# Performance work log

Hardware: AMD Instinct MI355X
Metric: run time of the kernel (lower is better)

The kernel has to match this reference:

```python
import jax, jax.numpy as jnp
import numpy as np

D = 512    # d_model == EMBED_DIM
H = 8      # nhead
FF = 2048  # dim_feedforward
T, B, S, M = 64, 32, 64, 256
EPS = 1e-5


def setup_inputs() -> dict:
    key = jax.random.key(0)
    ks = iter(jax.random.split(key, 40))
    rn = lambda k, shp, s=0.02: s * jax.random.normal(k, shp, jnp.float32)
    inp = {
        'tgt': jax.random.normal(next(ks), (T, B, D), jnp.float32),
        'memory': jax.random.normal(next(ks), (M, B, D), jnp.float32),
        'semantics': jax.random.normal(next(ks), (B, S, D), jnp.float32),
    }
    for pfx in ('pt', 'sa', 'ca'):  # pre_target, self_attn, cross multihead_attn
        inp[pfx + '_wqkv'] = rn(next(ks), (3 * D, D))
        inp[pfx + '_bqkv'] = jnp.zeros((3 * D,), jnp.float32)
        inp[pfx + '_wo'] = rn(next(ks), (D, D))
        inp[pfx + '_bo'] = jnp.zeros((D,), jnp.float32)
    # relevant_mlp_pre_target: fc0 (2D->D), relu, fc1 (D->D), relu, fc2 (D->1)
    inp['mlp_w0'] = rn(next(ks), (D, 2 * D), float(np.sqrt(2.0 / (2 * D))))
    inp['mlp_b0'] = jnp.zeros((D,), jnp.float32)
    inp['mlp_w1'] = rn(next(ks), (D, D), float(np.sqrt(2.0 / D)))
    inp['mlp_b1'] = jnp.zeros((D,), jnp.float32)
    inp['mlp_w2'] = rn(next(ks), (1, D), float(np.sqrt(2.0 / D)))
    inp['mlp_b2'] = jnp.zeros((1,), jnp.float32)
    inp['ffn_w1'] = rn(next(ks), (FF, D))
    inp['ffn_b1'] = jnp.zeros((FF,), jnp.float32)
    inp['ffn_w2'] = rn(next(ks), (D, FF))
    inp['ffn_b2'] = jnp.zeros((D,), jnp.float32)
    for i in (1, 2, 3):
        inp[f'ln{i}_g'] = jnp.ones((D,), jnp.float32)
        inp[f'ln{i}_b'] = jnp.zeros((D,), jnp.float32)
    return inp


def layernorm(x, g, b):
    mu = jnp.mean(x, -1, keepdims=True)
    var = jnp.var(x, -1, keepdims=True)
    return (x - mu) * jax.lax.rsqrt(var + EPS) * g + b


def mha(q, k, v, wqkv, bqkv, wo, bo):
    # q,k,v: (L, B, D) seq-first, like torch nn.MultiheadAttention
    hd = D // H
    wq, wk, wv = jnp.split(wqkv, 3, axis=0)
    bq, bk, bv = jnp.split(bqkv, 3)
    qh = (q @ wq.T + bq).reshape(q.shape[0], q.shape[1], H, hd)
    kh = (k @ wk.T + bk).reshape(k.shape[0], k.shape[1], H, hd)
    vh = (v @ wv.T + bv).reshape(v.shape[0], v.shape[1], H, hd)
    scale = 1.0 / float(np.sqrt(hd))
    att = jax.nn.softmax(jnp.einsum('qbhd,kbhd->bhqk', qh * scale, kh), axis=-1)
    out = jnp.einsum('bhqk,kbhd->qbhd', att, vh).reshape(q.shape[0], q.shape[1], D)
    return out @ wo.T + bo


def get_relevant_semantic(feats, sem, w0, b0, w1, b1, w2, b2):
    # feats: (B,T,D), sem: (B,S,D). Linear-on-concat == sum of two linears, so we
    # never materialize the (B,T,S,2D) cat tensor; hidden (B,T,S,D) is unavoidable math.
    w0c, w0s = w0[:, :D], w0[:, D:]
    h = (feats @ w0c.T)[:, :, None, :] + (sem @ w0s.T)[:, None, :, :] + b0  # (B,T,S,D)
    h = jax.nn.relu(h)
    h = jax.nn.relu(h @ w1.T + b1)
    scores = h @ w2.T + b2                      # (B,T,S,1)
    a = jax.nn.softmax(scores, axis=2)          # softmax over sem axis
    return jnp.sum(sem[:, None, :, :] * a, axis=2)  # (B,T,D)


def reference(tgt, memory, semantics,
              pt_wqkv, pt_bqkv, pt_wo, pt_bo,
              sa_wqkv, sa_bqkv, sa_wo, sa_bo,
              ca_wqkv, ca_bqkv, ca_wo, ca_bo,
              mlp_w0, mlp_b0, mlp_w1, mlp_b1, mlp_w2, mlp_b2,
              ffn_w1, ffn_b1, ffn_w2, ffn_b2,
              ln1_g, ln1_b, ln2_g, ln2_b, ln3_g, ln3_b):
    # MULTIHEAD_PRE_TARGET branch (eval mode: dropout = identity)
    rel = get_relevant_semantic(jnp.transpose(tgt, (1, 0, 2)), semantics,
                                mlp_w0, mlp_b0, mlp_w1, mlp_b1, mlp_w2, mlp_b2)
    sem_k = jnp.transpose(rel, (1, 0, 2))  # (T,B,D) seq-first key/value
    x = tgt + mha(tgt, sem_k, sem_k, pt_wqkv, pt_bqkv, pt_wo, pt_bo)
    # self attention
    x = layernorm(x + mha(x, x, x, sa_wqkv, sa_bqkv, sa_wo, sa_bo), ln1_g, ln1_b)
    # cross attention over encoder memory
    x = layernorm(x + mha(x, memory, memory, ca_wqkv, ca_bqkv, ca_wo, ca_bo), ln2_g, ln2_b)
    # feed-forward
    ff = jax.nn.relu(x @ ffn_w1.T + ffn_b1) @ ffn_w2.T + ffn_b2
    return layernorm(x + ff, ln3_g, ln3_b)
```

## Files before the change

kernel.cpp:

```cpp
#include <hip/hip_runtime.h>
#include <hip/hip_bf16.h>

#define WS_B 32

typedef __attribute__((ext_vector_type(8))) __bf16 bf16x8;
typedef __attribute__((ext_vector_type(4))) float f32x4;
typedef unsigned short ushort_t;

#define MB(x) ((size_t)(x) << 20)
#define LSTR 40

__device__ __forceinline__ unsigned packpair(float lo, float hi) {
    return ((__float_as_uint(lo) + 0x8000u) >> 16) |
           ((__float_as_uint(hi) + 0x8000u) & 0xffff0000u);
}
__device__ __forceinline__ ushort_t f2bf(float x) {
    return (ushort_t)((__float_as_uint(x) + 0x8000u) >> 16);
}
__device__ __forceinline__ float bf2f(ushort_t u) {
    return __uint_as_float(((unsigned)u) << 16);
}
__device__ __forceinline__ unsigned fuse_word(unsigned f, unsigned s) {
    float lo = __uint_as_float(f << 16) + __uint_as_float(s << 16);
    float hi = __uint_as_float(f & 0xffff0000u) + __uint_as_float(s & 0xffff0000u);
    lo = fmaxf(lo, 0.f);
    hi = fmaxf(hi, 0.f);
    return packpair(lo, hi);
}

struct CvtArgs {
    const float* src[13];
    ushort_t* dst[13];
    int n4[13];
};
__global__ __launch_bounds__(256) void megacvt_kernel(CvtArgs a) {
    const int t = blockIdx.y;
    const int n = a.n4[t];
    const float4* S = (const float4*)a.src[t];
    uint2* D = (uint2*)a.dst[t];
    for (int i = blockIdx.x * 256 + threadIdx.x; i < n; i += gridDim.x * 256) {
        float4 v = S[i];
        uint2 o;
        o.x = packpair(v.x, v.y);
        o.y = packpair(v.z, v.w);
        D[i] = o;
    }
}

struct GemmDesc {
    const ushort_t* A;
    const ushort_t* W;
    const float* bias;
    const float* resid;
    float* C;
    ushort_t* Cb;
    int lda, ldw, ldc, K, relu, nbx, blkStart;
};
struct GemmBatch {
    GemmDesc d[4];
    int nd;
};

__global__ __launch_bounds__(256, 3) void mfma_gemm2(GemmBatch bt) {
    __shared__ ushort_t As[128 * LSTR];
    __shared__ ushort_t Bs[128 * LSTR];
    int di = 0;
#pragma unroll
    for (int i = 1; i < 4; ++i)
        if (i < bt.nd && (int)blockIdx.x >= bt.d[i].blkStart) di = i;
    const GemmDesc g = bt.d[di];
    const int local = blockIdx.x - g.blkStart;
    const int mb = local / g.nbx;
    const int nb = local - mb * g.nbx;

    const int tid = threadIdx.x;
    const int w = tid >> 6, lane = tid & 63;
    const int wm = w & 1, wn = w >> 1;
    const int l15 = lane & 15, quad = lane >> 4;

    const int arow = tid >> 1;
    const int a16 = (tid & 1) * 16;
    const ushort_t* Ap = g.A + (long)(mb * 128 + arow) * g.lda + a16;
    const ushort_t* Bp = g.W + (long)(nb * 128 + arow) * g.ldw + a16;
    ushort_t* Asw = &As[arow * LSTR + a16];
    ushort_t* Bsw = &Bs[arow * LSTR + a16];

    f32x4 acc[4][4];
#pragma unroll
    for (int i = 0; i < 4; ++i)
#pragma unroll
        for (int j = 0; j < 4; ++j) acc[i][j] = (f32x4)0.f;

    uint4 a0 = *(const uint4*)Ap;
    uint4 a1 = *(const uint4*)(Ap + 8);
    uint4 b0 = *(const uint4*)Bp;
    uint4 b1 = *(const uint4*)(Bp + 8);

    for (int k0 = 0; k0 < g.K; k0 += 32) {
        __syncthreads();
        *(uint4*)Asw = a0; *(uint4*)(Asw + 8) = a1;
        *(uint4*)Bsw = b0; *(uint4*)(Bsw + 8) = b1;
        if (k0 + 32 < g.K) {
            a0 = *(const uint4*)(Ap + k0 + 32);
            a1 = *(const uint4*)(Ap + k0 + 40);
            b0 = *(const uint4*)(Bp + k0 + 32);
            b1 = *(const uint4*)(Bp + k0 + 40);
        }
        __syncthreads();
        bf16x8 af[4], bf[4];
#pragma unroll
        for (int mt = 0; mt < 4; ++mt)
            af[mt] = *(const bf16x8*)&As[(wm * 64 + mt * 16 + l15) * LSTR + quad * 8];
#pragma unroll
        for (int nt = 0; nt < 4; ++nt)
            bf[nt] = *(const bf16x8*)&Bs[(wn * 64 + nt * 16 + l15) * LSTR + quad * 8];
#pragma unroll
        for (int mt = 0; mt < 4; ++mt)
#pragma unroll
            for (int nt = 0; nt < 4; ++nt)
                acc[mt][nt] = __builtin_amdgcn_mfma_f32_16x16x32_bf16(
                    af[mt], bf[nt], acc[mt][nt], 0, 0, 0);
    }

#pragma unroll
    for (int nt = 0; nt < 4; ++nt) {
        const int col = nb * 128 + wn * 64 + nt * 16 + l15;
        const float bv = g.bias ? g.bias[col] : 0.f;
#pragma unroll
        for (int mt = 0; mt < 4; ++mt) {
            const int row0 = mb * 128 + wm * 64 + mt * 16 + quad * 4;
#pragma unroll
            for (int rg = 0; rg < 4; ++rg) {
                float v = acc[mt][nt][rg] + bv;
                if (g.relu) v = fmaxf(v, 0.f);
                const long off = (long)(row0 + rg) * g.ldc + col;
                if (g.resid) v += g.resid[off];
                if (g.C) g.C[off] = v;
                if (g.Cb) g.Cb[off] = f2bf(v);
            }
        }
    }
}

__global__ __launch_bounds__(512, 2) void h2score_kernel(
    const ushort_t* __restrict__ Fb,
    const ushort_t* __restrict__ Sb,
    const ushort_t* __restrict__ w1b,
    const float* __restrict__ b1,
    const float* __restrict__ w2,
    float* __restrict__ scores4)
{
    __shared__ ushort_t As[128 * LSTR];
    __shared__ ushort_t Bs[256 * LSTR];
    __shared__ float scred[128 * 4];
    const int tid = threadIdx.x;
    const int mb = blockIdx.x, nb = blockIdx.y;
    const int w = tid >> 6, lane = tid & 63;
    const int wm = w & 1, wn = w >> 1;
    const int l15 = lane & 15, quad = lane >> 4;

    const int arow = tid >> 2, akc = tid & 3;
    const int m_g = mb * 128 + arow;
    const int r = m_g >> 6, s = m_g & 63, bidx = r & 31;
    const ushort_t* Fp = Fb + (long)r * 512 + akc * 8;
    const ushort_t* Sp = Sb + (long)(bidx * 64 + s) * 512 + akc * 8;
    const ushort_t* Bp0 = w1b + (long)(nb * 256 + arow) * 512 + akc * 8;
    const ushort_t* Bp1 = Bp0 + (long)128 * 512;
    ushort_t* Asw  = &As[arow * LSTR + akc * 8];
    ushort_t* Bsw0 = &Bs[arow * LSTR + akc * 8];
    ushort_t* Bsw1 = Bsw0 + 128 * LSTR;

    f32x4 acc[4][4];
#pragma unroll
    for (int i = 0; i < 4; ++i)
#pragma unroll
        for (int j = 0; j < 4; ++j) acc[i][j] = (f32x4)0.f;

    uint4 fa = *(const uint4*)Fp;
    uint4 sa = *(const uint4*)Sp;
    uint4 bb0 = *(const uint4*)Bp0;
    uint4 bb1 = *(const uint4*)Bp1;

    for (int k0 = 0; k0 < 512; k0 += 32) {
        __syncthreads();
        uint4 o;
        o.x = fuse_word(fa.x, sa.x);
        o.y = fuse_word(fa.y, sa.y);
        o.z = fuse_word(fa.z, sa.z);
        o.w = fuse_word(fa.w, sa.w);
        *(uint4*)Asw = o;
        *(uint4*)Bsw0 = bb0;
        *(uint4*)Bsw1 = bb1;
        if (k0 + 32 < 512) {
            fa  = *(const uint4*)(Fp + k0 + 32);
            sa  = *(const uint4*)(Sp + k0 + 32);
            bb0 = *(const uint4*)(Bp0 + k0 + 32);
            bb1 = *(const uint4*)(Bp1 + k0 + 32);
        }
        __syncthreads();
        bf16x8 af[4], bf[4];
#pragma unroll
        for (int mt = 0; mt < 4; ++mt)
            af[mt] = *(const bf16x8*)&As[(wm * 64 + mt * 16 + l15) * LSTR + quad * 8];
#pragma unroll
        for (int nt = 0; nt < 4; ++nt)
            bf[nt] = *(const bf16x8*)&Bs[(wn * 64 + nt * 16 + l15) * LSTR + quad * 8];
#pragma unroll
        for (int mt = 0; mt < 4; ++mt)
#pragma unroll
            for (int nt = 0; nt < 4; ++nt)
                acc[mt][nt] = __builtin_amdgcn_mfma_f32_16x16x32_bf16(
                    af[mt], bf[nt], acc[mt][nt], 0, 0, 0);
    }
    __syncthreads();

    float sp[4][4];
#pragma unroll
    for (int mt = 0; mt < 4; ++mt)
#pragma unroll
        for (int rg = 0; rg < 4; ++rg) sp[mt][rg] = 0.f;
#pragma unroll
    for (int nt = 0; nt < 4; ++nt) {
        const int col = nb * 256 + wn * 64 + nt * 16 + l15;
        const float cb = b1[col];
        const float cw = w2[col];
#pragma unroll
        for (int mt = 0; mt < 4; ++mt) {
#pragma unroll
            for (int rg = 0; rg < 4; ++rg)
                sp[mt][rg] += fmaxf(acc[mt][nt][rg] + cb, 0.f) * cw;
        }
    }
#pragma unroll
    for (int mt = 0; mt < 4; ++mt)
#pragma unroll
        for (int rg = 0; rg < 4; ++rg) {
            float v = sp[mt][rg];
            v += __shfl_xor(v, 1);
            v += __shfl_xor(v, 2);
            v += __shfl_xor(v, 4);
            v += __shfl_xor(v, 8);
            if (l15 == 0)
                scred[(wm * 64 + mt * 16 + quad * 4 + rg) * 4 + wn] = v;
        }
    __syncthreads();
    if (tid < 128) {
        float t = scred[tid * 4] + scred[tid * 4 + 1]
                + scred[tid * 4 + 2] + scred[tid * 4 + 3];
        scores4[(long)nb * 131072 + mb * 128 + tid] = t;
    }
}

__global__ __launch_bounds__(256) void softrel_kernel(
    const float* __restrict__ sc4,
    const ushort_t* __restrict__ semb,
    ushort_t* __restrict__ rel)
{
    __shared__ float a_s[64];
    const int tid = threadIdx.x;
    const int r = blockIdx.x;
    const int b = r & (WS_B - 1);
    if (tid < 64) {
        float t = sc4[r * 64 + tid] + sc4[131072 + r * 64 + tid];
        float m = t;
#pragma unroll
        for (int off = 32; off > 0; off >>= 1) m = fmaxf(m, __shfl_xor(m, off));
        float e = __expf(t - m);
        float su = e;
#pragma unroll
        for (int off = 32; off > 0; off >>= 1) su += __shfl_xor(su, off);
        a_s[tid] = e / su;
    }
    __syncthreads();
#pragma unroll
    for (int dd = 0; dd < 2; ++dd) {
        const int d = tid + dd * 256;
        float accd = 0.f;
        const ushort_t* sp = semb + (long)b * 64 * 512 + d;
        for (int s = 0; s < 64; ++s)
            accd += a_s[s] * bf2f(sp[s * 512]);
        rel[(long)r * 512 + d] = f2bf(accd);
    }
}

__global__ __launch_bounds__(256) void attn2_kernel(
    const ushort_t* __restrict__ Qm, int ldq, int qoff,
    const ushort_t* __restrict__ Km, int ldk, int koff,
    const ushort_t* __restrict__ Vm, int ldv, int voff,
    ushort_t* __restrict__ O,
    int Lk)
{
    __shared__ float sQT[64 * 34];
    __shared__ float sKT[64 * 68];
    __shared__ float sS[32 * 260];
    __shared__ float sredm[8 * 34];
    __shared__ float sreds[8 * 34];
    const int tid = threadIdx.x;
    const int b  = blockIdx.x >> 4;
    const int h  = (blockIdx.x >> 1) & 7;
    const int qt = blockIdx.x & 1;
    const int L8 = Lk >> 3;

    {
        const int q = tid >> 3, c = tid & 7;
        const int qg = qt * 32 + q;
        const ushort_t* pp = Qm + (long)(qg * WS_B + b) * ldq + qoff + h * 64 + c * 8;
        uint4 u = *(const uint4*)pp;
        const ushort_t* us = (const ushort_t*)&u;
#pragma unroll
        for (int i = 0; i < 8; ++i)
            sQT[(c * 8 + i) * 34 + q] = bf2f(us[i]);
    }

    const int k4 = (tid & 15) * 4;
    const int q2 = (tid >> 4) * 2;

    for (int kt = 0; kt < Lk; kt += 64) {
        __syncthreads();
        {
            const int kk = tid >> 3, c = tid & 7;
#pragma unroll
            for (int half = 0; half < 2; ++half) {
                const int kr = kk + half * 32;
                const ushort_t* pp = Km + (long)((kt + kr) * WS_B + b) * ldk + koff + h * 64 + c * 8;
                uint4 u = *(const uint4*)pp;
                const ushort_t* us = (const ushort_t*)&u;
#pragma unroll
                for (int i = 0; i < 8; ++i)
                    sKT[(c * 8 + i) * 68 + kr] = bf2f(us[i]);
            }
        }
        __syncthreads();
        float acc[2][4] = {{0.f, 0.f, 0.f, 0.f}, {0.f, 0.f, 0.f, 0.f}};
        for (int d = 0; d < 64; ++d) {
            const float qa = sQT[d * 34 + q2];
            const float qb = sQT[d * 34 + q2 + 1];
            const float4 kv = *(const float4*)&sKT[d * 68 + k4];
            acc[0][0] += qa * kv.x; acc[0][1] += qa * kv.y;
            acc[0][2] += qa * kv.z; acc[0][3] += qa * kv.w;
            acc[1][0] += qb * kv.x; acc[1][1] += qb * kv.y;
            acc[1][2] += qb * kv.z; acc[1][3] += qb * kv.w;
        }
#pragma unroll
        for (int i = 0; i < 2; ++i) {
            float4 v;
            v.x = acc[i][0] * 0.125f; v.y = acc[i][1] * 0.125f;
            v.z = acc[i][2] * 0.125f; v.w = acc[i][3] * 0.125f;
            *(float4*)&sS[(q2 + i) * 260 + kt + k4] = v;
        }
    }
    __syncthreads();

    {
        const int q = tid & 31, part = tid >> 5;
        const int kb = part * L8;
        float m = -1e30f;
        for (int k = 0; k < L8; ++k) m = fmaxf(m, sS[q * 260 + kb + k]);
        sredm[part * 34 + q] = m;
        __syncthreads();
        float M = sredm[q];
#pragma unroll
        for (int pz = 1; pz < 8; ++pz) M = fmaxf(M, sredm[pz * 34 + q]);
        float su = 0.f;
        for (int k = 0; k < L8; ++k) {
            float e = __expf(sS[q * 260 + kb + k] - M);
            sS[q * 260 + kb + k] = e;
            su += e;
        }
        sreds[part * 34 + q] = su;
    }
    __syncthreads();

    const int d4 = (tid & 15) * 4;
    float o[2][4] = {{0.f, 0.f, 0.f, 0.f}, {0.f, 0.f, 0.f, 0.f}};
    float* sV = sKT;
    for (int kt = 0; kt < Lk; kt += 64) {
        __syncthreads();
        {
            const int kk = tid >> 3, c = tid & 7;
#pragma unroll
            for (int half = 0; half < 2; ++half) {
                const int kr = kk + half * 32;
                const ushort_t* pp = Vm + (long)((kt + kr) * WS_B + b) * ldv + voff + h * 64 + c * 8;
                uint4 u = *(const uint4*)pp;
                const ushort_t* us = (const ushort_t*)&u;
                float4 w0, w1;
                w0.x = bf2f(us[0]); w0.y = bf2f(us[1]);
                w0.z = bf2f(us[2]); w0.w = bf2f(us[3]);
                w1.x = bf2f(us[4]); w1.y = bf2f(us[5]);
                w1.z = bf2f(us[6]); w1.w = bf2f(us[7]);
                *(float4*)&sV[kr * 68 + c * 8] = w0;
                *(float4*)&sV[kr * 68 + c * 8 + 4] = w1;
            }
        }
        __syncthreads();
        for (int k = 0; k < 64; ++k) {
            const float p0 = sS[q2 * 260 + kt + k];
            const float p1 = sS[(q2 + 1) * 260 + kt + k];
            const float4 vv = *(const float4*)&sV[k * 68 + d4];
            o[0][0] += p0 * vv.x; o[0][1] += p0 * vv.y;
            o[0][2] += p0 * vv.z; o[0][3] += p0 * vv.w;
            o[1][0] += p1 * vv.x; o[1][1] += p1 * vv.y;
            o[1][2] += p1 * vv.z; o[1][3] += p1 * vv.w;
        }
    }

#pragma unroll
    for (int i = 0; i < 2; ++i) {
        float su = 0.f;
#pragma unroll
        for (int pz = 0; pz < 8; ++pz) su += sreds[pz * 34 + q2 + i];
        const float inv = 1.f / su;
        const int qg = qt * 32 + q2 + i;
        ushort_t* op = O + (long)(qg * WS_B + b) * 512 + h * 64 + d4;
        uint2 pk;
        pk.x = packpair(o[i][0] * inv, o[i][1] * inv);
        pk.y = packpair(o[i][2] * inv, o[i][3] * inv);
        *(uint2*)op = pk;
    }
}

__global__ __launch_bounds__(256) void ln_kernel(
    const float* __restrict__ X,
    const float* __restrict__ g,
    const float* __restrict__ be,
    float* __restrict__ Y,
    ushort_t* __restrict__ Yb)
{
    const int row = blockIdx.x * 4 + (threadIdx.x >> 6);
    const int lane = threadIdx.x & 63;
    const float4* xp = (const float4*)(X + (long)row * 512);
    float4 x0 = xp[lane], x1 = xp[lane + 64];
    float sum = x0.x + x0.y + x0.z + x0.w + x1.x + x1.y + x1.z + x1.w;
    float sq = x0.x * x0.x + x0.y * x0.y + x0.z * x0.z + x0.w * x0.w
             + x1.x * x1.x + x1.y * x1.y + x1.z * x1.z + x1.w * x1.w;
#pragma unroll
    for (int off = 32; off > 0; off >>= 1) {
        sum += __shfl_xor(sum, off);
        sq += __shfl_xor(sq, off);
    }
    const float mu = sum * (1.f / 512.f);
    const float var = sq * (1.f / 512.f) - mu * mu;
    const float rs = rsqrtf(var + 1e-5f);
    const float4* gp = (const float4*)g;
    const float4* bp = (const float4*)be;
    float4 g0 = gp[lane], g1 = gp[lane + 64], b0 = bp[lane], b1 = bp[lane + 64];
    float4 y0, y1;
    y0.x = (x0.x - mu) * rs * g0.x + b0.x;
    y0.y = (x0.y - mu) * rs * g0.y + b0.y;
    y0.z = (x0.z - mu) * rs * g0.z + b0.z;
    y0.w = (x0.w - mu) * rs * g0.w + b0.w;
    y1.x = (x1.x - mu) * rs * g1.x + b1.x;
    y1.y = (x1.y - mu) * rs * g1.y + b1.y;
    y1.z = (x1.z - mu) * rs * g1.z + b1.z;
    y1.w = (x1.w - mu) * rs * g1.w + b1.w;
    float4* yp = (float4*)(Y + (long)row * 512);
    yp[lane] = y0; yp[lane + 64] = y1;
    if (Yb) {
        uint2* ybp = (uint2*)(Yb + (long)row * 512);
        uint2 p0, p1;
        p0.x = packpair(y0.x, y0.y); p0.y = packpair(y0.z, y0.w);
        p1.x = packpair(y1.x, y1.y); p1.y = packpair(y1.z, y1.w);
        ybp[lane] = p0; ybp[lane + 64] = p1;
    }
}

static inline GemmDesc mkdesc(const ushort_t* A, int lda, const ushort_t* W, int ldw,
                              const float* bias, const float* resid, float* C,
                              ushort_t* Cb, int ldc, int N, int K, int relu,
                              int blkStart)
{
    GemmDesc d;
    d.A = A; d.W = W; d.bias = bias; d.resid = resid; d.C = C; d.Cb = Cb;
    d.lda = lda; d.ldw = ldw; d.ldc = ldc; d.K = K; d.relu = relu;
    d.nbx = N / 128;
    d.blkStart = blkStart;
    return d;
}
static inline void mgemm(hipStream_t s, const ushort_t* A, int lda,
                         const ushort_t* W, int ldw, const float* bias,
                         const float* resid, float* C, ushort_t* Cb,
                         int ldc, int M, int N, int K, bool relu)
{
    GemmBatch bt;
    bt.nd = 1;
    bt.d[0] = mkdesc(A, lda, W, ldw, bias, resid, C, Cb, ldc, N, K, relu ? 1 : 0, 0);
    bt.d[1] = bt.d[0]; bt.d[2] = bt.d[0]; bt.d[3] = bt.d[0];
    mfma_gemm2<<<(M / 128) * (N / 128), 256, 0, s>>>(bt);
}

extern "C" void kernel_launch(void* const* d_in, const int* in_sizes, int n_in,
                              void* d_out, int out_size, void* d_ws, size_t ws_size,
                              hipStream_t stream)
{
    (void)in_sizes; (void)n_in; (void)out_size; (void)ws_size;
    const float* tgt       = (const float*)d_in[0];
    const float* memory    = (const float*)d_in[1];
    const float* semantics = (const float*)d_in[2];
    const float* pt_wqkv   = (const float*)d_in[3];
    const float* pt_bqkv   = (const float*)d_in[4];
    const float* pt_wo     = (const float*)d_in[5];
    const float* pt_bo     = (const float*)d_in[6];
    const float* sa_wqkv   = (const float*)d_in[7];
    const float* sa_bqkv   = (const float*)d_in[8];
    const float* sa_wo     = (const float*)d_in[9];
    const float* sa_bo     = (const float*)d_in[10];
    const float* ca_wqkv   = (const float*)d_in[11];
    const float* ca_bqkv   = (const float*)d_in[12];
    const float* ca_wo     = (const float*)d_in[13];
    const float* ca_bo     = (const float*)d_in[14];
    const float* mlp_w0    = (const float*)d_in[15];
    const float* mlp_b0    = (const float*)d_in[16];
    const float* mlp_w1    = (const float*)d_in[17];
    const float* mlp_b1    = (const float*)d_in[18];
    const float* mlp_w2    = (const float*)d_in[19];
    const float* ffn_w1    = (const float*)d_in[21];
    const float* ffn_b1    = (const float*)d_in[22];
    const float* ffn_w2    = (const float*)d_in[23];
    const float* ffn_b2    = (const float*)d_in[24];
    const float* ln1_g     = (const float*)d_in[25];
    const float* ln1_b     = (const float*)d_in[26];
    const float* ln2_g     = (const float*)d_in[27];
    const float* ln2_b     = (const float*)d_in[28];
    const float* ln3_g     = (const float*)d_in[29];
    const float* ln3_b     = (const float*)d_in[30];

    char* p = (char*)d_ws;
    ushort_t* w0b   = (ushort_t*)(p + 0);
    ushort_t* w1b   = (ushort_t*)(p + MB(1));
    ushort_t* ptwb  = (ushort_t*)(p + 1572864);
    ushort_t* ptob  = (ushort_t*)(p + MB(3));
    ushort_t* sawb  = (ushort_t*)(p + 3670016);
    ushort_t* saob  = (ushort_t*)(p + MB(5));
    ushort_t* cawb  = (ushort_t*)(p + 5767168);
    ushort_t* caob  = (ushort_t*)(p + MB(7));
    ushort_t* f1b   = (ushort_t*)(p + 7864320);
    ushort_t* f2b   = (ushort_t*)(p + 9961472);
    ushort_t* memb  = (ushort_t*)(p + MB(12));
    ushort_t* cakvb = (ushort_t*)(p + MB(20));
    ushort_t* tgtb  = (ushort_t*)(p + MB(36));
    ushort_t* semb  = (ushort_t*)(p + MB(38));
    ushort_t* Fb    = (ushort_t*)(p + MB(40));
    ushort_t* Sb    = (ushort_t*)(p + MB(42));
    float*    scores4 = (float*)(p + MB(44));
    ushort_t* relb  = (ushort_t*)(p + MB(45));
    ushort_t* Ob    = (ushort_t*)(p + MB(47));
    float*    x1f   = (float*)(p + MB(49));
    ushort_t* ptqb  = (ushort_t*)(p + MB(53));
    ushort_t* ptkvb = (ushort_t*)(p + MB(14));
    ushort_t* x1b   = (ushort_t*)(p + MB(18));
    ushort_t* saqkvb= (ushort_t*)(p + MB(38));
    float*    yf    = (float*)(p + MB(12));
    float*    x2f   = (float*)(p + MB(16));
    ushort_t* x2b   = (ushort_t*)(p + MB(36));
    ushort_t* caqb  = (ushort_t*)(p + MB(44));
    float*    x3f   = (float*)(p + MB(40));
    ushort_t* x3b   = (ushort_t*)(p + MB(38));
    ushort_t* hb    = (ushort_t*)(p + MB(20));

    CvtArgs ca;
    ca.src[0]  = tgt;       ca.dst[0]  = tgtb;  ca.n4[0]  = 262144;
    ca.src[1]  = semantics; ca.dst[1]  = semb;  ca.n4[1]  = 262144;
    ca.src[2]  = memory;    ca.dst[2]  = memb;  ca.n4[2]  = 1048576;
    ca.src[3]  = mlp_w0;    ca.dst[3]  = w0b;   ca.n4[3]  = 131072;
    ca.src[4]  = mlp_w1;    ca.dst[4]  = w1b;   ca.n4[4]  = 65536;
    ca.src[5]  = pt_wqkv;   ca.dst[5]  = ptwb;  ca.n4[5]  = 196608;
    ca.src[6]  = pt_wo;     ca.dst[6]  = ptob;  ca.n4[6]  = 65536;
    ca.src[7]  = sa_wqkv;   ca.dst[7]  = sawb;  ca.n4[7]  = 196608;
    ca.src[8]  = sa_wo;     ca.dst[8]  = saob;  ca.n4[8]  = 65536;
    ca.src[9]  = ca_wqkv;   ca.dst[9]  = cawb;  ca.n4[9]  = 196608;
    ca.src[10] = ca_wo;     ca.dst[10] = caob;  ca.n4[10] = 65536;
    ca.src[11] = ffn_w1;    ca.dst[11] = f1b;   ca.n4[11] = 262144;
    ca.src[12] = ffn_w2;    ca.dst[12] = f2b;   ca.n4[12] = 262144;
    megacvt_kernel<<<dim3(1024, 13), 256, 0, stream>>>(ca);

    {
        GemmBatch bt;
        bt.nd = 4;
        bt.d[0] = mkdesc(memb, 512, cawb + 512 * 512, 512, ca_bqkv + 512, nullptr,
                         nullptr, cakvb, 1024, 1024, 512, 0, 0);
        bt.d[1] = mkdesc(tgtb, 512, w0b, 1024, mlp_b0, nullptr,
                         nullptr, Fb, 512, 512, 512, 0, 512);
        bt.d[2] = mkdesc(semb, 512, w0b + 512, 1024, nullptr, nullptr,
                         nullptr, Sb, 512, 512, 512, 0, 576);
        bt.d[3] = mkdesc(tgtb, 512, ptwb, 512, pt_bqkv, nullptr,
                         nullptr, ptqb, 512, 512, 512, 0, 640);
        mfma_gemm2<<<704, 256, 0, stream>>>(bt);
    }

    h2score_kernel<<<dim3(1024, 2), 512, 0, stream>>>(Fb, Sb, w1b, mlp_b1,
                                                      mlp_w2, scores4);
    softrel_kernel<<<2048, 256, 0, stream>>>(scores4, semb, relb);

    mgemm(stream, relb, 512, ptwb + 512 * 512, 512, pt_bqkv + 512, nullptr,
          nullptr, ptkvb, 1024, 2048, 1024, 512, false);
    attn2_kernel<<<512, 256, 0, stream>>>(ptqb, 512, 0, ptkvb, 1024, 0,
                                          ptkvb, 1024, 512, Ob, 64);
    mgemm(stream, Ob, 512, ptob, 512, pt_bo, tgt, x1f, x1b, 512,
          2048, 512, 512, false);

    mgemm(stream, x1b, 512, sawb, 512, sa_bqkv, nullptr, nullptr, saqkvb, 1536,
          2048, 1536, 512, false);
    attn2_kernel<<<512, 256, 0, stream>>>(saqkvb, 1536, 0, saqkvb, 1536, 512,
                                          saqkvb, 1536, 1024, Ob, 64);
    mgemm(stream, Ob, 512, saob, 512, sa_bo, x1f, yf, nullptr, 512,
          2048, 512, 512, false);
    ln_kernel<<<512, 256, 0, stream>>>(yf, ln1_g, ln1_b, x2f, x2b);

    mgemm(stream, x2b, 512, cawb, 512, ca_bqkv, nullptr, nullptr, caqb, 512,
          2048, 512, 512, false);
    attn2_kernel<<<512, 256, 0, stream>>>(caqb, 512, 0, cakvb, 1024, 0,
                                          cakvb, 1024, 512, Ob, 256);
    mgemm(stream, Ob, 512, caob, 512, ca_bo, x2f, yf, nullptr, 512,
          2048, 512, 512, false);
    ln_kernel<<<512, 256, 0, stream>>>(yf, ln2_g, ln2_b, x3f, x3b);

    mgemm(stream, x3b, 512, f1b, 512, ffn_b1, nullptr, nullptr, hb, 2048,
          2048, 2048, 512, true);
    mgemm(stream, hb, 2048, f2b, 2048, ffn_b2, x3f, yf, nullptr, 512,
          2048, 512, 2048, false);
    ln_kernel<<<512, 256, 0, stream>>>(yf, ln3_g, ln3_b, (float*)d_out, nullptr);
}
```

Before: 527.7 us.

## Fuse MLP score GEMM with softmax and relevance reduction in one kernel

The h2score kernel now computes the full 512-wide hidden layer per 128-row block (8 N-tiles per wave) instead of splitting N across two blocks. This lets it reduce scores, apply the softmax over the 64 semantics, and compute the weighted semantic sum in the same kernel, removing the scores4 round-trip and the separate softrel launch. LDS row stride also drops from padded 40 to unpadded 32 in both GEMMs, which may add bank conflicts. The doubled accumulator count raises register pressure and halves the grid, which can lower occupancy.

```diff
diff --git a/kernel.cpp b/kernel.cpp
--- a/kernel.cpp
+++ b/kernel.cpp
@@ -8,7 +8,6 @@
 typedef unsigned short ushort_t;
 
 #define MB(x) ((size_t)(x) << 20)
-#define LSTR 40
 
 __device__ __forceinline__ unsigned packpair(float lo, float hi) {
     return ((__float_as_uint(lo) + 0x8000u) >> 16) |
@@ -62,8 +61,8 @@
 };
 
 __global__ __launch_bounds__(256, 3) void mfma_gemm2(GemmBatch bt) {
-    __shared__ ushort_t As[128 * LSTR];
-    __shared__ ushort_t Bs[128 * LSTR];
+    __shared__ ushort_t As[128 * 32];
+    __shared__ ushort_t Bs[128 * 32];
     int di = 0;
 #pragma unroll
     for (int i = 1; i < 4; ++i)
@@ -82,8 +81,8 @@
     const int a16 = (tid & 1) * 16;
     const ushort_t* Ap = g.A + (long)(mb * 128 + arow) * g.lda + a16;
     const ushort_t* Bp = g.W + (long)(nb * 128 + arow) * g.ldw + a16;
-    ushort_t* Asw = &As[arow * LSTR + a16];
-    ushort_t* Bsw = &Bs[arow * LSTR + a16];
+    ushort_t* Asw = &As[arow * 32 + a16];
+    ushort_t* Bsw = &Bs[arow * 32 + a16];
 
     f32x4 acc[4][4];
 #pragma unroll
@@ -110,10 +109,10 @@
         bf16x8 af[4], bf[4];
 #pragma unroll
         for (int mt = 0; mt < 4; ++mt)
-            af[mt] = *(const bf16x8*)&As[(wm * 64 + mt * 16 + l15) * LSTR + quad * 8];
+            af[mt] = *(const bf16x8*)&As[(wm * 64 + mt * 16 + l15) * 32 + quad * 8];
 #pragma unroll
         for (int nt = 0; nt < 4; ++nt)
-            bf[nt] = *(const bf16x8*)&Bs[(wn * 64 + nt * 16 + l15) * LSTR + quad * 8];
+            bf[nt] = *(const bf16x8*)&Bs[(wn * 64 + nt * 16 + l15) * 32 + quad * 8];
 #pragma unroll
         for (int mt = 0; mt < 4; ++mt)
 #pragma unroll
@@ -142,19 +141,19 @@
     }
 }
 
-__global__ __launch_bounds__(512, 2) void h2score_kernel(
+__global__ __launch_bounds__(512) void h2rel_kernel(
     const ushort_t* __restrict__ Fb,
     const ushort_t* __restrict__ Sb,
     const ushort_t* __restrict__ w1b,
     const float* __restrict__ b1,
     const float* __restrict__ w2,
-    float* __restrict__ scores4)
+    const ushort_t* __restrict__ semb,
+    ushort_t* __restrict__ relb)
 {
-    __shared__ ushort_t As[128 * LSTR];
-    __shared__ ushort_t Bs[256 * LSTR];
-    __shared__ float scred[128 * 4];
+    __shared__ ushort_t As[128 * 32];
+    __shared__ ushort_t Bs[512 * 32];
     const int tid = threadIdx.x;
-    const int mb = blockIdx.x, nb = blockIdx.y;
+    const int mb = blockIdx.x;
     const int w = tid >> 6, lane = tid & 63;
     const int wm = w & 1, wn = w >> 1;
     const int l15 = lane & 15, quad = lane >> 4;
@@ -164,22 +163,22 @@
     const int r = m_g >> 6, s = m_g & 63, bidx = r & 31;
     const ushort_t* Fp = Fb + (long)r * 512 + akc * 8;
     const ushort_t* Sp = Sb + (long)(bidx * 64 + s) * 512 + akc * 8;
-    const ushort_t* Bp0 = w1b + (long)(nb * 256 + arow) * 512 + akc * 8;
-    const ushort_t* Bp1 = Bp0 + (long)128 * 512;
-    ushort_t* Asw  = &As[arow * LSTR + akc * 8];
-    ushort_t* Bsw0 = &Bs[arow * LSTR + akc * 8];
-    ushort_t* Bsw1 = Bsw0 + 128 * LSTR;
-
-    f32x4 acc[4][4];
+    const ushort_t* Bp = w1b + (long)arow * 512 + akc * 8;
+    ushort_t* Asw = &As[arow * 32 + akc * 8];
+    ushort_t* Bsw = &Bs[arow * 32 + akc * 8];
+
+    f32x4 acc[4][8];
 #pragma unroll
     for (int i = 0; i < 4; ++i)
 #pragma unroll
-        for (int j = 0; j < 4; ++j) acc[i][j] = (f32x4)0.f;
+        for (int j = 0; j < 8; ++j) acc[i][j] = (f32x4)0.f;
 
     uint4 fa = *(const uint4*)Fp;
     uint4 sa = *(const uint4*)Sp;
-    uint4 bb0 = *(const uint4*)Bp0;
-    uint4 bb1 = *(const uint4*)Bp1;
+    uint4 bb[4];
+#pragma unroll
+    for (int j = 0; j < 4; ++j)
+        bb[j] = *(const uint4*)(Bp + (long)j * 128 * 512);
 
     for (int k0 = 0; k0 < 512; k0 += 32) {
         __syncthreads();
@@ -189,26 +188,30 @@
         o.z = fuse_word(fa.z, sa.z);
         o.w = fuse_word(fa.w, sa.w);
         *(uint4*)Asw = o;
-        *(uint4*)Bsw0 = bb0;
-        *(uint4*)Bsw1 = bb1;
+#pragma unroll
+        for (int j = 0; j < 4; ++j)
+            *(uint4*)(Bsw + j * 128 * 32) = bb[j];
         if (k0 + 32 < 512) {
-            fa  = *(const uint4*)(Fp + k0 + 32);
-            sa  = *(const uint4*)(Sp + k0 + 32);
-            bb0 = *(const uint4*)(Bp0 + k0 + 32);
-            bb1 = *(const uint4*)(Bp1 + k0 + 32);
-        }
-        __syncthreads();
-        bf16x8 af[4], bf[4];
+            fa = *(const uint4*)(Fp + k0 + 32);
+            sa = *(const uint4*)(Sp + k0 + 32);
+#pragma unroll
+            for (int j = 0; j < 4; ++j)
+                bb[j] = *(const uint4*)(Bp + (long)j * 128 * 512 + k0 + 32);
+        }
+        __syncthreads();
+        bf16x8 af[4], bf[8];
 #pragma unroll
         for (int mt = 0; mt < 4; ++mt)
-            af[mt] = *(const bf16x8*)&As[(wm * 64 + mt * 16 + l15) * LSTR + quad * 8];
-#pragma unroll
-        for (int nt = 0; nt < 4; ++nt)
-            bf[nt] = *(const bf16x8*)&Bs[(wn * 64 + nt * 16 + l15) * LSTR + quad * 8];
+            af[mt] = *(const bf16x8*)&As[(wm * 64 + mt * 16 + l15) * 32 + quad * 8];
+#pragma unroll
+        for (int nt = 0; nt < 8; ++nt) {
+            const int brow = (nt >> 2) * 256 + wn * 64 + (nt & 3) * 16 + l15;
+            bf[nt] = *(const bf16x8*)&Bs[brow * 32 + quad * 8];
+        }
 #pragma unroll
         for (int mt = 0; mt < 4; ++mt)
 #pragma unroll
-            for (int nt = 0; nt < 4; ++nt)
+            for (int nt = 0; nt < 8; ++nt)
                 acc[mt][nt] = __builtin_amdgcn_mfma_f32_16x16x32_bf16(
                     af[mt], bf[nt], acc[mt][nt], 0, 0, 0);
     }
@@ -220,8 +223,8 @@
 #pragma unroll
         for (int rg = 0; rg < 4; ++rg) sp[mt][rg] = 0.f;
 #pragma unroll
-    for (int nt = 0; nt < 4; ++nt) {
-        const int col = nb * 256 + wn * 64 + nt * 16 + l15;
+    for (int nt = 0; nt < 8; ++nt) {
+        const int col = (nt >> 2) * 256 + wn * 64 + (nt & 3) * 16 + l15;
         const float cb = b1[col];
         const float cw = w2[col];
 #pragma unroll
@@ -231,6 +234,7 @@
                 sp[mt][rg] += fmaxf(acc[mt][nt][rg] + cb, 0.f) * cw;
         }
     }
+    float* scred = (float*)As;
 #pragma unroll
     for (int mt = 0; mt < 4; ++mt)
 #pragma unroll
@@ -244,42 +248,42 @@
                 scred[(wm * 64 + mt * 16 + quad * 4 + rg) * 4 + wn] = v;
         }
     __syncthreads();
+
+    float* sm = ((float*)As) + 512;
+    if (tid < 128)
+        sm[tid] = scred[tid * 4] + scred[tid * 4 + 1]
+                + scred[tid * 4 + 2] + scred[tid * 4 + 3];
+    __syncthreads();
+
+    float* aw = ((float*)As) + 640;
     if (tid < 128) {
-        float t = scred[tid * 4] + scred[tid * 4 + 1]
-                + scred[tid * 4 + 2] + scred[tid * 4 + 3];
-        scores4[(long)nb * 131072 + mb * 128 + tid] = t;
-    }
-}
-
-__global__ __launch_bounds__(256) void softrel_kernel(
-    const float* __restrict__ sc4,
-    const ushort_t* __restrict__ semb,
-    ushort_t* __restrict__ rel)
-{
-    __shared__ float a_s[64];
-    const int tid = threadIdx.x;
-    const int r = blockIdx.x;
-    const int b = r & (WS_B - 1);
-    if (tid < 64) {
-        float t = sc4[r * 64 + tid] + sc4[131072 + r * 64 + tid];
-        float m = t;
-#pragma unroll
-        for (int off = 32; off > 0; off >>= 1) m = fmaxf(m, __shfl_xor(m, off));
-        float e = __expf(t - m);
+        float t = sm[tid];
+        float mx = t;
+#pragma unroll
+        for (int off = 32; off > 0; off >>= 1) mx = fmaxf(mx, __shfl_xor(mx, off));
+        float e = __expf(t - mx);
         float su = e;
 #pragma unroll
         for (int off = 32; off > 0; off >>= 1) su += __shfl_xor(su, off);
-        a_s[tid] = e / su;
+        aw[tid] = e / su;
     }
     __syncthreads();
-#pragma unroll
-    for (int dd = 0; dd < 2; ++dd) {
-        const int d = tid + dd * 256;
-        float accd = 0.f;
-        const ushort_t* sp = semb + (long)b * 64 * 512 + d;
-        for (int s = 0; s < 64; ++s)
-            accd += a_s[s] * bf2f(sp[s * 512]);
-        rel[(long)r * 512 + d] = f2bf(accd);
+
+    {
+        const int rhalf = tid >> 8;
+        const int d2 = (tid & 255) * 2;
+        const int rr = mb * 2 + rhalf;
+        const int bb2 = rr & 31;
+        const float* a = aw + rhalf * 64;
+        const ushort_t* sp2 = semb + (long)bb2 * 64 * 512 + d2;
+        float a0 = 0.f, a1 = 0.f;
+        for (int s2 = 0; s2 < 64; ++s2) {
+            const unsigned u = *(const unsigned*)(sp2 + s2 * 512);
+            const float wgt = a[s2];
+            a0 += wgt * __uint_as_float(u << 16);
+            a1 += wgt * __uint_as_float(u & 0xffff0000u);
+        }
+        *(unsigned*)(relb + (long)rr * 512 + d2) = packpair(a0, a1);
     }
 }
 
@@ -542,7 +546,6 @@
     ushort_t* semb  = (ushort_t*)(p + MB(38));
     ushort_t* Fb    = (ushort_t*)(p + MB(40));
     ushort_t* Sb    = (ushort_t*)(p + MB(42));
-    float*    scores4 = (float*)(p + MB(44));
     ushort_t* relb  = (ushort_t*)(p + MB(45));
     ushort_t* Ob    = (ushort_t*)(p + MB(47));
     float*    x1f   = (float*)(p + MB(49));
@@ -588,9 +591,7 @@
         mfma_gemm2<<<704, 256, 0, stream>>>(bt);
     }
 
-    h2score_kernel<<<dim3(1024, 2), 512, 0, stream>>>(Fb, Sb, w1b, mlp_b1,
-                                                      mlp_w2, scores4);
-    softrel_kernel<<<2048, 256, 0, stream>>>(scores4, semb, relb);
+    h2rel_kernel<<<1024, 512, 0, stream>>>(Fb, Sb, w1b, mlp_b1, mlp_w2, semb, relb);
 
     mgemm(stream, relb, 512, ptwb + 512 * 512, 512, pt_bqkv + 512, nullptr,
           nullptr, ptkvb, 1024, 2048, 1024, 512, false);
```

After: 626.8 us. +18.8%, slower.

## Add 64x128 two-wave GEMM kernel for standalone GEMMs and drop LDS padding

Applied to the files above, without the earlier changes.

Adds a new GEMM kernel that uses 128-thread blocks, each computing a 64x128 tile, and routes every standalone GEMM launch through it, doubling the number of blocks so the 2048-row GEMMs fill more compute units. It also removes the 40-element LDS row padding, switching to an unpadded 32-element stride in all GEMM kernels, which likely introduces LDS bank conflicts on the fragment reads. The h2score kernel stops prefetching the next K-slice into registers and loads it inside the loop instead, giving up load/compute overlap in exchange for fewer live registers.

```diff
diff --git a/kernel.cpp b/kernel.cpp
--- a/kernel.cpp
+++ b/kernel.cpp
@@ -8,7 +8,6 @@
 typedef unsigned short ushort_t;
 
 #define MB(x) ((size_t)(x) << 20)
-#define LSTR 40
 
 __device__ __forceinline__ unsigned packpair(float lo, float hi) {
     return ((__float_as_uint(lo) + 0x8000u) >> 16) |
@@ -62,8 +61,8 @@
 };
 
 __global__ __launch_bounds__(256, 3) void mfma_gemm2(GemmBatch bt) {
-    __shared__ ushort_t As[128 * LSTR];
-    __shared__ ushort_t Bs[128 * LSTR];
+    __shared__ ushort_t As[128 * 32];
+    __shared__ ushort_t Bs[128 * 32];
     int di = 0;
 #pragma unroll
     for (int i = 1; i < 4; ++i)
@@ -82,8 +81,8 @@
     const int a16 = (tid & 1) * 16;
     const ushort_t* Ap = g.A + (long)(mb * 128 + arow) * g.lda + a16;
     const ushort_t* Bp = g.W + (long)(nb * 128 + arow) * g.ldw + a16;
-    ushort_t* Asw = &As[arow * LSTR + a16];
-    ushort_t* Bsw = &Bs[arow * LSTR + a16];
+    ushort_t* Asw = &As[arow * 32 + a16];
+    ushort_t* Bsw = &Bs[arow * 32 + a16];
 
     f32x4 acc[4][4];
 #pragma unroll
@@ -110,10 +109,10 @@
         bf16x8 af[4], bf[4];
 #pragma unroll
         for (int mt = 0; mt < 4; ++mt)
-            af[mt] = *(const bf16x8*)&As[(wm * 64 + mt * 16 + l15) * LSTR + quad * 8];
+            af[mt] = *(const bf16x8*)&As[(wm * 64 + mt * 16 + l15) * 32 + quad * 8];
 #pragma unroll
         for (int nt = 0; nt < 4; ++nt)
-            bf[nt] = *(const bf16x8*)&Bs[(wn * 64 + nt * 16 + l15) * LSTR + quad * 8];
+            bf[nt] = *(const bf16x8*)&Bs[(wn * 64 + nt * 16 + l15) * 32 + quad * 8];
 #pragma unroll
         for (int mt = 0; mt < 4; ++mt)
 #pragma unroll
@@ -142,6 +141,90 @@
     }
 }
 
+__global__ __launch_bounds__(128, 3) void mfma_gemm3(GemmBatch bt) {
+    __shared__ ushort_t As[64 * 32];
+    __shared__ ushort_t Bs[128 * 32];
+    int di = 0;
+#pragma unroll
+    for (int i = 1; i < 4; ++i)
+        if (i < bt.nd && (int)blockIdx.x >= bt.d[i].blkStart) di = i;
+    const GemmDesc g = bt.d[di];
+    const int local = blockIdx.x - g.blkStart;
+    const int mb = local / g.nbx;
+    const int nb = local - mb * g.nbx;
+
+    const int tid = threadIdx.x;
+    const int wn = tid >> 6, lane = tid & 63;
+    const int l15 = lane & 15, quad = lane >> 4;
+
+    const int ar = tid >> 1, ac = (tid & 1) * 16;
+    const ushort_t* Ap = g.A + (long)(mb * 64 + ar) * g.lda + ac;
+    const ushort_t* Bp = g.W + (long)(nb * 128 + tid) * g.ldw;
+    ushort_t* Asw = &As[ar * 32 + ac];
+    ushort_t* Bsw = &Bs[tid * 32];
+
+    f32x4 acc[4][4];
+#pragma unroll
+    for (int i = 0; i < 4; ++i)
+#pragma unroll
+        for (int j = 0; j < 4; ++j) acc[i][j] = (f32x4)0.f;
+
+    uint4 a0 = *(const uint4*)Ap;
+    uint4 a1 = *(const uint4*)(Ap + 8);
+    uint4 b0 = *(const uint4*)Bp;
+    uint4 b1 = *(const uint4*)(Bp + 8);
+    uint4 b2 = *(const uint4*)(Bp + 16);
+    uint4 b3 = *(const uint4*)(Bp + 24);
+
+    for (int k0 = 0; k0 < g.K; k0 += 32) {
+        __syncthreads();
+        *(uint4*)Asw = a0; *(uint4*)(Asw + 8) = a1;
+        *(uint4*)Bsw = b0; *(uint4*)(Bsw + 8) = b1;
+        *(uint4*)(Bsw + 16) = b2; *(uint4*)(Bsw + 24) = b3;
+        if (k0 + 32 < g.K) {
+            a0 = *(const uint4*)(Ap + k0 + 32);
+            a1 = *(const uint4*)(Ap + k0 + 40);
+            b0 = *(const uint4*)(Bp + k0 + 32);
+            b1 = *(const uint4*)(Bp + k0 + 40);
+            b2 = *(const uint4*)(Bp + k0 + 48);
+            b3 = *(const uint4*)(Bp + k0 + 56);
+        }
+        __syncthreads();
+        bf16x8 af[4], bf[4];
+#pragma unroll
+        for (int mt = 0; mt < 4; ++mt)
+            af[mt] = *(const bf16x8*)&As[(mt * 16 + l15) * 32 + quad * 8];
+#pragma unroll
+        for (int nt = 0; nt < 4; ++nt)
+            bf[nt] = *(const bf16x8*)&Bs[(wn * 64 + nt * 16 + l15) * 32 + quad * 8];
+#pragma unroll
+        for (int mt = 0; mt < 4; ++mt)
+#pragma unroll
+            for (int nt = 0; nt < 4; ++nt)
+                acc[mt][nt] = __builtin_amdgcn_mfma_f32_16x16x32_bf16(
+                    af[mt], bf[nt], acc[mt][nt], 0, 0, 0);
+    }
+
+#pragma unroll
+    for (int nt = 0; nt < 4; ++nt) {
+        const int col = nb * 128 + wn * 64 + nt * 16 + l15;
+        const float bv = g.bias ? g.bias[col] : 0.f;
+#pragma unroll
+        for (int mt = 0; mt < 4; ++mt) {
+            const int row0 = mb * 64 + mt * 16 + quad * 4;
+#pragma unroll
+            for (int rg = 0; rg < 4; ++rg) {
+                float v = acc[mt][nt][rg] + bv;
+                if (g.relu) v = fmaxf(v, 0.f);
+                const long off = (long)(row0 + rg) * g.ldc + col;
+                if (g.resid) v += g.resid[off];
+                if (g.C) g.C[off] = v;
+                if (g.Cb) g.Cb[off] = f2bf(v);
+            }
+        }
+    }
+}
+
 __global__ __launch_bounds__(512, 2) void h2score_kernel(
     const ushort_t* __restrict__ Fb,
     const ushort_t* __restrict__ Sb,
@@ -150,8 +233,8 @@
     const float* __restrict__ w2,
     float* __restrict__ scores4)
 {
-    __shared__ ushort_t As[128 * LSTR];
-    __shared__ ushort_t Bs[256 * LSTR];
+    __shared__ ushort_t As[128 * 32];
+    __shared__ ushort_t Bs[256 * 32];
     __shared__ float scred[128 * 4];
     const int tid = threadIdx.x;
     const int mb = blockIdx.x, nb = blockIdx.y;
@@ -166,9 +249,9 @@
     const ushort_t* Sp = Sb + (long)(bidx * 64 + s) * 512 + akc * 8;
     const ushort_t* Bp0 = w1b + (long)(nb * 256 + arow) * 512 + akc * 8;
     const ushort_t* Bp1 = Bp0 + (long)128 * 512;
-    ushort_t* Asw  = &As[arow * LSTR + akc * 8];
-    ushort_t* Bsw0 = &Bs[arow * LSTR + akc * 8];
-    ushort_t* Bsw1 = Bsw0 + 128 * LSTR;
+    ushort_t* Asw = &As[arow * 32 + akc * 8];
+    ushort_t* Bsw0 = &Bs[arow * 32 + akc * 8];
+    ushort_t* Bsw1 = Bsw0 + 128 * 32;
 
     f32x4 acc[4][4];
 #pragma unroll
@@ -176,12 +259,11 @@
 #pragma unroll
         for (int j = 0; j < 4; ++j) acc[i][j] = (f32x4)0.f;
 
-    uint4 fa = *(const uint4*)Fp;
-    uint4 sa = *(const uint4*)Sp;
-    uint4 bb0 = *(const uint4*)Bp0;
-    uint4 bb1 = *(const uint4*)Bp1;
-
     for (int k0 = 0; k0 < 512; k0 += 32) {
+        uint4 fa = *(const uint4*)(Fp + k0);
+        uint4 sa = *(const uint4*)(Sp + k0);
+        uint4 bb0 = *(const uint4*)(Bp0 + k0);
+        uint4 bb1 = *(const uint4*)(Bp1 + k0);
         __syncthreads();
         uint4 o;
         o.x = fuse_word(fa.x, sa.x);
@@ -191,20 +273,14 @@
         *(uint4*)Asw = o;
         *(uint4*)Bsw0 = bb0;
         *(uint4*)Bsw1 = bb1;
-        if (k0 + 32 < 512) {
-            fa  = *(const uint4*)(Fp + k0 + 32);
-            sa  = *(const uint4*)(Sp + k0 + 32);
-            bb0 = *(const uint4*)(Bp0 + k0 + 32);
-            bb1 = *(const uint4*)(Bp1 + k0 + 32);
-        }
         __syncthreads();
         bf16x8 af[4], bf[4];
 #pragma unroll
         for (int mt = 0; mt < 4; ++mt)
-            af[mt] = *(const bf16x8*)&As[(wm * 64 + mt * 16 + l15) * LSTR + quad * 8];
+            af[mt] = *(const bf16x8*)&As[(wm * 64 + mt * 16 + l15) * 32 + quad * 8];
 #pragma unroll
         for (int nt = 0; nt < 4; ++nt)
-            bf[nt] = *(const bf16x8*)&Bs[(wn * 64 + nt * 16 + l15) * LSTR + quad * 8];
+            bf[nt] = *(const bf16x8*)&Bs[(wn * 64 + nt * 16 + l15) * 32 + quad * 8];
 #pragma unroll
         for (int mt = 0; mt < 4; ++mt)
 #pragma unroll
@@ -477,16 +553,16 @@
     d.blkStart = blkStart;
     return d;
 }
-static inline void mgemm(hipStream_t s, const ushort_t* A, int lda,
-                         const ushort_t* W, int ldw, const float* bias,
-                         const float* resid, float* C, ushort_t* Cb,
-                         int ldc, int M, int N, int K, bool relu)
+static inline void mgemm3(hipStream_t s, const ushort_t* A, int lda,
+                          const ushort_t* W, int ldw, const float* bias,
+                          const float* resid, float* C, ushort_t* Cb,
+                          int ldc, int M, int N, int K, bool relu)
 {
     GemmBatch bt;
     bt.nd = 1;
     bt.d[0] = mkdesc(A, lda, W, ldw, bias, resid, C, Cb, ldc, N, K, relu ? 1 : 0, 0);
     bt.d[1] = bt.d[0]; bt.d[2] = bt.d[0]; bt.d[3] = bt.d[0];
-    mfma_gemm2<<<(M / 128) * (N / 128), 256, 0, s>>>(bt);
+    mfma_gemm3<<<(M / 64) * (N / 128), 128, 0, s>>>(bt);
 }
 
 extern "C" void kernel_launch(void* const* d_in, const int* in_sizes, int n_in,
@@ -592,32 +668,32 @@
                                                       mlp_w2, scores4);
     softrel_kernel<<<2048, 256, 0, stream>>>(scores4, semb, relb);
 
-    mgemm(stream, relb, 512, ptwb + 512 * 512, 512, pt_bqkv + 512, nullptr,
-          nullptr, ptkvb, 1024, 2048, 1024, 512, false);
+    mgemm3(stream, relb, 512, ptwb + 512 * 512, 512, pt_bqkv + 512, nullptr,
+           nullptr, ptkvb, 1024, 2048, 1024, 512, false);
     attn2_kernel<<<512, 256, 0, stream>>>(ptqb, 512, 0, ptkvb, 1024, 0,
                                           ptkvb, 1024, 512, Ob, 64);
-    mgemm(stream, Ob, 512, ptob, 512, pt_bo, tgt, x1f, x1b, 512,
-          2048, 512, 512, false);
-
-    mgemm(stream, x1b, 512, sawb, 512, sa_bqkv, nullptr, nullptr, saqkvb, 1536,
-          2048, 1536, 512, false);
+    mgemm3(stream, Ob, 512, ptob, 512, pt_bo, tgt, x1f, x1b, 512,
+           2048, 512, 512, false);
+
+    mgemm3(stream, x1b, 512, sawb, 512, sa_bqkv, nullptr, nullptr, saqkvb, 1536,
+           2048, 1536, 512, false);
     attn2_kernel<<<512, 256, 0, stream>>>(saqkvb, 1536, 0, saqkvb, 1536, 512,
                                           saqkvb, 1536, 1024, Ob, 64);
-    mgemm(stream, Ob, 512, saob, 512, sa_bo, x1f, yf, nullptr, 512,
-          2048, 512, 512, false);
+    mgemm3(stream, Ob, 512, saob, 512, sa_bo, x1f, yf, nullptr, 512,
+           2048, 512, 512, false);
     ln_kernel<<<512, 256, 0, stream>>>(yf, ln1_g, ln1_b, x2f, x2b);
 
-    mgemm(stream, x2b, 512, cawb, 512, ca_bqkv, nullptr, nullptr, caqb, 512,
-          2048, 512, 512, false);
+    mgemm3(stream, x2b, 512, cawb, 512, ca_bqkv, nullptr, nullptr, caqb, 512,
+           2048, 512, 512, false);
     attn2_kernel<<<512, 256, 0, stream>>>(caqb, 512, 0, cakvb, 1024, 0,
                                           cakvb, 1024, 512, Ob, 256);
-    mgemm(stream, Ob, 512, caob, 512, ca_bo, x2f, yf, nullptr, 512,
-          2048, 512, 512, false);
+    mgemm3(stream, Ob, 512, caob, 512, ca_bo, x2f, yf, nullptr, 512,
+           2048, 512, 512, false);
     ln_kernel<<<512, 256, 0, stream>>>(yf, ln2_g, ln2_b, x3f, x3b);
 
-    mgemm(stream, x3b, 512, f1b, 512, ffn_b1, nullptr, nullptr, hb, 2048,
-          2048, 2048, 512, true);
-    mgemm(stream, hb, 2048, f2b, 2048, ffn_b2, x3f, yf, nullptr, 512,
-          2048, 512, 2048, false);
+    mgemm3(stream, x3b, 512, f1b, 512, ffn_b1, nullptr, nullptr, hb, 2048,
+           2048, 2048, 512, true);
+    mgemm3(stream, hb, 2048, f2b, 2048, ffn_b2, x3f, yf, nullptr, 512,
+           2048, 512, 2048, false);
     ln_kernel<<<512, 256, 0, stream>>>(yf, ln3_g, ln3_b, (float*)d_out, nullptr);
 }
```

Result: no change. 520.6 us (-1.3%).
